# Kernel tuning notes

Measured on AMD Instinct MI355X. Metric: run time of the kernel, lower is better.

The kernel has to match this reference:

```python
import jax, jax.numpy as jnp
import numpy as np

B, S, D, E, K = 2, 4096, 1024, 8, 2

def setup_inputs() -> dict:
    key = jax.random.key(0)
    k1, k2, k3, k4, k5 = jax.random.split(key, 5)
    x = jax.random.normal(k1, (B, S, D), dtype=jnp.float32)
    expert_weights = jax.random.uniform(k2, (B, S, K), dtype=jnp.float32)
    top_k_indices = jax.random.randint(k3, (B, S, K), 0, E, dtype=jnp.int32)
    W = jax.random.normal(k4, (E, D, D), dtype=jnp.float32) * (1.0 / np.sqrt(D))
    b = jax.random.normal(k5, (E, D), dtype=jnp.float32) * 0.01
    return {"x": x, "expert_weights": expert_weights,
            "top_k_indices": top_k_indices, "W": W, "b": b}

def reference(x, expert_weights, top_k_indices, W, b):
    # Dense all-expert linear: [B,S,E,Dout]
    expert_outputs = jnp.einsum('bsd,edf->bsef', x, W) + b  # bias broadcasts over b,s
    # Gather the top-k expert outputs per token: [B,S,K,Dout]
    gathered = jnp.take_along_axis(expert_outputs, top_k_indices[:, :, :, None], axis=2)
    # Weighted combine over k
    output = jnp.sum(expert_weights[:, :, :, None] * gathered, axis=2)
    return output
```

## Files before the change

kernel.cpp:

```cpp
#include <hip/hip_runtime.h>
#include <hip/hip_bf16.h>
#include <cstdio>
#include <cstdint>

static constexpr int TOK = 8192;
static constexpr int DIM = 1024;
static constexpr int NEXP = 8;
static constexpr int NGRP = 16;
static constexpr int ROWS = TOK * 2;

typedef unsigned short u16;
typedef unsigned int u32;

using floatx4 = __attribute__((ext_vector_type(4))) float;
using bf16x8  = __attribute__((ext_vector_type(8))) __bf16;


__device__ __forceinline__ u16 f2bf(float f) {
  union { float f; u32 u; } v; v.f = f;
  u32 r = v.u + 0x7fffu + ((v.u >> 16) & 1u);
  return (u16)(r >> 16);
}

__device__ __forceinline__ float bf2f(u16 b) {
  union { u32 u; float f; } v; v.u = (u32)b << 16;
  return v.f;
}

__device__ __forceinline__ void gload_lds16(const void* g, void* l) {
  __builtin_amdgcn_global_load_lds(
      (const __attribute__((address_space(1))) void*)g,
      (__attribute__((address_space(3))) void*)l,
      16, 0, 0);
}

__global__ __launch_bounds__(1024)
void prep_kernel(const int* __restrict__ idx, const float* __restrict__ ew,
                 int* __restrict__ meta, int* __restrict__ tileMap,
                 int* __restrict__ tokList, float* __restrict__ wList) {
  __shared__ int cnt[NGRP];
  __shared__ int curL[NGRP];
  const int tid = threadIdx.x;
  if (tid < NGRP) cnt[tid] = 0;
  __syncthreads();
  int gloc[16];
#pragma unroll
  for (int j = 0; j < 16; ++j) {
    int i = tid + 1024 * j;
    int e = idx[i];
    int g = ((i & 1) << 3) | e;
    gloc[j] = g;
    atomicAdd(&cnt[g], 1);
  }
  __syncthreads();
  if (tid == 0) {
    int run = 0, t = 0, tk0 = 0;
    for (int g = 0; g < NGRP; ++g) {
      curL[g] = run;
      meta[g] = cnt[g];
      meta[16 + g] = run;
      int ntl = (cnt[g] + 127) >> 7;
      for (int m0 = 0; m0 < ntl; ++m0) tileMap[t++] = (g << 12) | m0;
      if (g == NEXP - 1) tk0 = t;
      run += cnt[g];
    }
    meta[48] = t;
    meta[49] = tk0;
  }
  __syncthreads();
#pragma unroll
  for (int j = 0; j < 16; ++j) {
    int i = tid + 1024 * j;
    int pos = atomicAdd(&curL[gloc[j]], 1);
    tokList[pos] = i >> 1;
    wList[pos] = ew[i];
  }
}

__global__ __launch_bounds__(256)
void gather_x_kernel(const float* __restrict__ x, const int* __restrict__ tokList,
                     u16* __restrict__ Abuf) {
  const int row = blockIdx.x;
  const int tok = tokList[row];
  const int tid = threadIdx.x;
  float4 v = reinterpret_cast<const float4*>(x + ((size_t)tok << 10))[tid];
  ushort4 o;
  o.x = f2bf(v.x); o.y = f2bf(v.y); o.z = f2bf(v.z); o.w = f2bf(v.w);
  reinterpret_cast<ushort4*>(Abuf + ((size_t)row << 10))[tid] = o;
}

__global__ void transpose_w_kernel(const float* __restrict__ W, u16* __restrict__ wt) {
  __shared__ u16 tile[32][33];
  const int e = blockIdx.z;
  const int f0 = blockIdx.x * 32, d0 = blockIdx.y * 32;
  const float* src = W + ((size_t)e << 20);
  u16* dst = wt + ((size_t)e << 20);
  const int tx = threadIdx.x, ty = threadIdx.y;
#pragma unroll
  for (int j = 0; j < 4; ++j) {
    int d = d0 + ty + 8 * j;
    tile[ty + 8 * j][tx] = f2bf(src[(size_t)d * DIM + f0 + tx]);
  }
  __syncthreads();
#pragma unroll
  for (int j = 0; j < 4; ++j) {
    int f = f0 + ty + 8 * j;
    dst[(size_t)f * DIM + d0 + tx] = tile[tx][ty + 8 * j];
  }
}

__global__ __launch_bounds__(256)
void moe_gemm_kernel(const u16* __restrict__ Abuf, const u16* __restrict__ wt,
                     const float* __restrict__ bias, const int* __restrict__ tokList,
                     const float* __restrict__ wList, const int* __restrict__ meta,
                     const int* __restrict__ tileMap, float* __restrict__ out,
                     u16* __restrict__ cbuf, int pass) {
  constexpr int BM = 128, BN = 128, BK = 64;
  const int chunk = gridDim.y;
  int lin = blockIdx.y * 8 + blockIdx.x;
  int swz = (lin & 7) * chunk + (lin >> 3);
  int tileIdx = swz >> 3, nt = swz & 7;

  int tBase = 0, tEnd = meta[48];
  const int tilesK0 = meta[49];
  if (pass == 0) tEnd = tilesK0;
  else if (pass == 1) tBase = tilesK0;
  tileIdx += tBase;
  if (tileIdx >= tEnd) return;

  const int tm = tileMap[tileIdx];
  const int g = tm >> 12, m0 = tm & 0xfff;
  const int e = g & (NEXP - 1);
  const int nrem = meta[g] - m0 * BM;
  const int listBase = meta[16 + g] + m0 * BM;

  __shared__ __align__(16) u16 As[BM * BK];
  __shared__ __align__(16) u16 Bs[BN * BK];

  const int tid = threadIdx.x;
  const int rowA = tid >> 3;
  const int chnk = tid & 7;
  const u16* wb = wt + ((size_t)e << 20);
  const u16* ab = Abuf + ((size_t)listBase << 10);

  const int wid = tid >> 6, lane = tid & 63;
  const int wm = (wid >> 1) * 64, wn = (wid & 1) * 64;
  const int lr = lane & 15, lg = lane >> 4;

  floatx4 acc[4][4];
#pragma unroll
  for (int i = 0; i < 4; ++i)
#pragma unroll
    for (int j = 0; j < 4; ++j) acc[i][j] = (floatx4){0.f, 0.f, 0.f, 0.f};

  for (int kt = 0; kt < DIM / BK; ++kt) {
    __syncthreads();
#pragma unroll
    for (int r = 0; r < 4; ++r) {
      const int row = rowA + 32 * r;
      gload_lds16(ab + ((size_t)row << 10) + kt * BK + chnk * 8,
                  &As[row * BK + chnk * 8]);
    }
#pragma unroll
    for (int r = 0; r < 4; ++r) {
      const int row = rowA + 32 * r;
      gload_lds16(wb + ((size_t)(nt * BN + row) << 10) + kt * BK + chnk * 8,
                  &Bs[row * BK + chnk * 8]);
    }
    asm volatile("s_waitcnt vmcnt(0)" ::: "memory");
    __syncthreads();

#pragma unroll
    for (int ks = 0; ks < 2; ++ks) {
      bf16x8 av[4], bv[4];
#pragma unroll
      for (int mi = 0; mi < 4; ++mi)
        av[mi] = *reinterpret_cast<const bf16x8*>(&As[(wm + mi * 16 + lr) * BK + ks * 32 + lg * 8]);
#pragma unroll
      for (int ni = 0; ni < 4; ++ni)
        bv[ni] = *reinterpret_cast<const bf16x8*>(&Bs[(wn + ni * 16 + lr) * BK + ks * 32 + lg * 8]);
#pragma unroll
      for (int mi = 0; mi < 4; ++mi)
#pragma unroll
        for (int ni = 0; ni < 4; ++ni)
          acc[mi][ni] = __builtin_amdgcn_mfma_f32_16x16x32_bf16(av[mi], bv[ni], acc[mi][ni], 0, 0, 0);
    }
  }

  const bool toCbuf = (pass < 0) && (g >= NEXP);
  const bool rmw = (pass == 1);
  const float* bp = bias + e * DIM;
#pragma unroll
  for (int mi = 0; mi < 4; ++mi) {
#pragma unroll
    for (int r = 0; r < 4; ++r) {
      const int rl = wm + mi * 16 + lg * 4 + r;
      if (rl < nrem) {
        const int   tok = tokList[listBase + rl];
        const float w   = wList[listBase + rl];
        const size_t rowOff = (size_t)tok << 10;
#pragma unroll
        for (int ni = 0; ni < 4; ++ni) {
          const int col = nt * BN + wn + ni * 16 + lr;
          const float v = w * (acc[mi][ni][r] + bp[col]);
          if (toCbuf)      cbuf[rowOff + col] = f2bf(v);
          else if (rmw)    out[rowOff + col] += v;
          else             out[rowOff + col] = v;
        }
      }
    }
  }
}

__global__ __launch_bounds__(256)
void combine_kernel(float* __restrict__ out, const u16* __restrict__ cbuf) {
  const int p = blockIdx.x * 256 + threadIdx.x;
  uint4 c = reinterpret_cast<const uint4*>(cbuf)[p];
  float4* o4 = reinterpret_cast<float4*>(out) + 2 * (size_t)p;
  float4 a = o4[0], b = o4[1];
  a.x += bf2f((u16)(c.x & 0xffff)); a.y += bf2f((u16)(c.x >> 16));
  a.z += bf2f((u16)(c.y & 0xffff)); a.w += bf2f((u16)(c.y >> 16));
  b.x += bf2f((u16)(c.z & 0xffff)); b.y += bf2f((u16)(c.z >> 16));
  b.z += bf2f((u16)(c.w & 0xffff)); b.w += bf2f((u16)(c.w >> 16));
  o4[0] = a; o4[1] = b;
}

extern "C" void kernel_launch(void* const* d_in, const int* in_sizes, int n_in,
                              void* d_out, int out_size, void* d_ws, size_t ws_size,
                              hipStream_t stream) {
  const float* x    = (const float*)d_in[0];
  const float* ew   = (const float*)d_in[1];
  const int*   idx  = (const int*)d_in[2];
  const float* W    = (const float*)d_in[3];
  const float* bias = (const float*)d_in[4];
  float* out = (float*)d_out;

  char* ws = (char*)d_ws;
  u16*   Abuf = (u16*)ws;
  u16*   wtp  = (u16*)(ws + ((size_t)32 << 20));
  u16*   cbuf = (u16*)(ws + ((size_t)48 << 20));

  const size_t needB = ((size_t)48 << 20) + (132 << 10);
  const size_t needA = ((size_t)64 << 20) + (132 << 10);
  if (ws_size < needB) {
    fprintf(stderr, "kernel_launch: ws_size %zu < needed %zu\n", ws_size, needB);
    return;
  }
  const bool modeA = (ws_size >= needA);
  char* tail = ws + (modeA ? ((size_t)64 << 20) : ((size_t)48 << 20));
  int*   tokList = (int*)tail;
  float* wList   = (float*)(tail + (64 << 10));
  int*   meta    = (int*)(tail + (128 << 10));
  int*   tileMap = (int*)(tail + (129 << 10));

  prep_kernel<<<1, 1024, 0, stream>>>(idx, ew, meta, tileMap, tokList, wList);
  gather_x_kernel<<<ROWS, 256, 0, stream>>>(x, tokList, Abuf);
  transpose_w_kernel<<<dim3(32, 32, 8), dim3(32, 8), 0, stream>>>(W, wtp);

  if (modeA) {
    moe_gemm_kernel<<<dim3(8, 144), 256, 0, stream>>>(
        Abuf, wtp, bias, tokList, wList, meta, tileMap, out, cbuf, -1);
    combine_kernel<<<TOK * DIM / 8 / 256, 256, 0, stream>>>(out, cbuf);
  } else {
    moe_gemm_kernel<<<dim3(8, 72), 256, 0, stream>>>(
        Abuf, wtp, bias, tokList, wList, meta, tileMap, out, nullptr, 0);
    moe_gemm_kernel<<<dim3(8, 72), 256, 0, stream>>>(
        Abuf, wtp, bias, tokList, wList, meta, tileMap, out, nullptr, 1);
  }
}
```

Baseline: 137.1 us.

## Replace two-pass combine with atomic-add epilogue and scatter-based gather

```diff
diff --git a/kernel.cpp b/kernel.cpp
--- a/kernel.cpp
+++ b/kernel.cpp
@@ -22,11 +22,6 @@
   return (u16)(r >> 16);
 }
 
-__device__ __forceinline__ float bf2f(u16 b) {
-  union { u32 u; float f; } v; v.u = (u32)b << 16;
-  return v.f;
-}
-
 __device__ __forceinline__ void gload_lds16(const void* g, void* l) {
   __builtin_amdgcn_global_load_lds(
       (const __attribute__((address_space(1))) void*)g,
@@ -37,56 +32,57 @@
 __global__ __launch_bounds__(1024)
 void prep_kernel(const int* __restrict__ idx, const float* __restrict__ ew,
                  int* __restrict__ meta, int* __restrict__ tileMap,
-                 int* __restrict__ tokList, float* __restrict__ wList) {
-  __shared__ int cnt[NGRP];
-  __shared__ int curL[NGRP];
+                 int* __restrict__ tokList, float* __restrict__ wList,
+                 int* __restrict__ posOf) {
+  __shared__ int cnt[NGRP], offS[NGRP], cur[NGRP], tbase[NGRP];
   const int tid = threadIdx.x;
   if (tid < NGRP) cnt[tid] = 0;
   __syncthreads();
-  int gloc[16];
+  int gl[16];
 #pragma unroll
   for (int j = 0; j < 16; ++j) {
     int i = tid + 1024 * j;
-    int e = idx[i];
-    int g = ((i & 1) << 3) | e;
-    gloc[j] = g;
+    int g = ((i & 1) << 3) | idx[i];
+    gl[j] = g;
     atomicAdd(&cnt[g], 1);
   }
   __syncthreads();
   if (tid == 0) {
-    int run = 0, t = 0, tk0 = 0;
+    int run = 0, t = 0;
     for (int g = 0; g < NGRP; ++g) {
-      curL[g] = run;
-      meta[g] = cnt[g];
-      meta[16 + g] = run;
-      int ntl = (cnt[g] + 127) >> 7;
-      for (int m0 = 0; m0 < ntl; ++m0) tileMap[t++] = (g << 12) | m0;
-      if (g == NEXP - 1) tk0 = t;
+      offS[g] = run; cur[g] = run; tbase[g] = t;
+      t += (cnt[g] + 127) >> 7;
       run += cnt[g];
     }
     meta[48] = t;
-    meta[49] = tk0;
-  }
-  __syncthreads();
+  }
+  __syncthreads();
+  if (tid < NGRP) {
+    meta[tid] = cnt[tid];
+    meta[16 + tid] = offS[tid];
+    int b = tbase[tid], n = (cnt[tid] + 127) >> 7;
+    for (int m0 = 0; m0 < n; ++m0) tileMap[b + m0] = (tid << 12) | m0;
+  }
 #pragma unroll
   for (int j = 0; j < 16; ++j) {
     int i = tid + 1024 * j;
-    int pos = atomicAdd(&curL[gloc[j]], 1);
+    int pos = atomicAdd(&cur[gl[j]], 1);
     tokList[pos] = i >> 1;
     wList[pos] = ew[i];
+    posOf[i] = pos;
   }
 }
 
 __global__ __launch_bounds__(256)
-void gather_x_kernel(const float* __restrict__ x, const int* __restrict__ tokList,
+void gather_x_kernel(const float* __restrict__ x, const int* __restrict__ posOf,
                      u16* __restrict__ Abuf) {
-  const int row = blockIdx.x;
-  const int tok = tokList[row];
-  const int tid = threadIdx.x;
-  float4 v = reinterpret_cast<const float4*>(x + ((size_t)tok << 10))[tid];
+  const int t = blockIdx.x, tid = threadIdx.x;
+  float4 v = reinterpret_cast<const float4*>(x + ((size_t)t << 10))[tid];
   ushort4 o;
   o.x = f2bf(v.x); o.y = f2bf(v.y); o.z = f2bf(v.z); o.w = f2bf(v.w);
-  reinterpret_cast<ushort4*>(Abuf + ((size_t)row << 10))[tid] = o;
+  const int p0 = posOf[2 * t], p1 = posOf[2 * t + 1];
+  reinterpret_cast<ushort4*>(Abuf + ((size_t)p0 << 10))[tid] = o;
+  reinterpret_cast<ushort4*>(Abuf + ((size_t)p1 << 10))[tid] = o;
 }
 
 __global__ void transpose_w_kernel(const float* __restrict__ W, u16* __restrict__ wt) {
@@ -110,23 +106,24 @@
 }
 
 __global__ __launch_bounds__(256)
+void zero_out_kernel(float4* __restrict__ out) {
+  const int i = blockIdx.x * 256 + threadIdx.x;
+#pragma unroll
+  for (int j = 0; j < 4; ++j)
+    out[i + j * 524288] = (float4){0.f, 0.f, 0.f, 0.f};
+}
+
+__global__ __launch_bounds__(256)
 void moe_gemm_kernel(const u16* __restrict__ Abuf, const u16* __restrict__ wt,
                      const float* __restrict__ bias, const int* __restrict__ tokList,
                      const float* __restrict__ wList, const int* __restrict__ meta,
-                     const int* __restrict__ tileMap, float* __restrict__ out,
-                     u16* __restrict__ cbuf, int pass) {
+                     const int* __restrict__ tileMap, float* __restrict__ out) {
   constexpr int BM = 128, BN = 128, BK = 64;
   const int chunk = gridDim.y;
   int lin = blockIdx.y * 8 + blockIdx.x;
   int swz = (lin & 7) * chunk + (lin >> 3);
   int tileIdx = swz >> 3, nt = swz & 7;
-
-  int tBase = 0, tEnd = meta[48];
-  const int tilesK0 = meta[49];
-  if (pass == 0) tEnd = tilesK0;
-  else if (pass == 1) tBase = tilesK0;
-  tileIdx += tBase;
-  if (tileIdx >= tEnd) return;
+  if (tileIdx >= meta[48]) return;
 
   const int tm = tileMap[tileIdx];
   const int g = tm >> 12, m0 = tm & 0xfff;
@@ -187,8 +184,6 @@
     }
   }
 
-  const bool toCbuf = (pass < 0) && (g >= NEXP);
-  const bool rmw = (pass == 1);
   const float* bp = bias + e * DIM;
 #pragma unroll
   for (int mi = 0; mi < 4; ++mi) {
@@ -198,31 +193,15 @@
       if (rl < nrem) {
         const int   tok = tokList[listBase + rl];
         const float w   = wList[listBase + rl];
-        const size_t rowOff = (size_t)tok << 10;
+        float* orow = out + ((size_t)tok << 10);
 #pragma unroll
         for (int ni = 0; ni < 4; ++ni) {
           const int col = nt * BN + wn + ni * 16 + lr;
-          const float v = w * (acc[mi][ni][r] + bp[col]);
-          if (toCbuf)      cbuf[rowOff + col] = f2bf(v);
-          else if (rmw)    out[rowOff + col] += v;
-          else             out[rowOff + col] = v;
+          unsafeAtomicAdd(&orow[col], w * (acc[mi][ni][r] + bp[col]));
         }
       }
     }
   }
-}
-
-__global__ __launch_bounds__(256)
-void combine_kernel(float* __restrict__ out, const u16* __restrict__ cbuf) {
-  const int p = blockIdx.x * 256 + threadIdx.x;
-  uint4 c = reinterpret_cast<const uint4*>(cbuf)[p];
-  float4* o4 = reinterpret_cast<float4*>(out) + 2 * (size_t)p;
-  float4 a = o4[0], b = o4[1];
-  a.x += bf2f((u16)(c.x & 0xffff)); a.y += bf2f((u16)(c.x >> 16));
-  a.z += bf2f((u16)(c.y & 0xffff)); a.w += bf2f((u16)(c.y >> 16));
-  b.x += bf2f((u16)(c.z & 0xffff)); b.y += bf2f((u16)(c.z >> 16));
-  b.z += bf2f((u16)(c.w & 0xffff)); b.w += bf2f((u16)(c.w >> 16));
-  o4[0] = a; o4[1] = b;
 }
 
 extern "C" void kernel_launch(void* const* d_in, const int* in_sizes, int n_in,
@@ -238,33 +217,23 @@
   char* ws = (char*)d_ws;
   u16*   Abuf = (u16*)ws;
   u16*   wtp  = (u16*)(ws + ((size_t)32 << 20));
-  u16*   cbuf = (u16*)(ws + ((size_t)48 << 20));
-
-  const size_t needB = ((size_t)48 << 20) + (132 << 10);
-  const size_t needA = ((size_t)64 << 20) + (132 << 10);
-  if (ws_size < needB) {
-    fprintf(stderr, "kernel_launch: ws_size %zu < needed %zu\n", ws_size, needB);
-    return;
-  }
-  const bool modeA = (ws_size >= needA);
-  char* tail = ws + (modeA ? ((size_t)64 << 20) : ((size_t)48 << 20));
+  char*  tail = ws + ((size_t)48 << 20);
   int*   tokList = (int*)tail;
   float* wList   = (float*)(tail + (64 << 10));
-  int*   meta    = (int*)(tail + (128 << 10));
-  int*   tileMap = (int*)(tail + (129 << 10));
-
-  prep_kernel<<<1, 1024, 0, stream>>>(idx, ew, meta, tileMap, tokList, wList);
-  gather_x_kernel<<<ROWS, 256, 0, stream>>>(x, tokList, Abuf);
+  int*   posOf   = (int*)(tail + (128 << 10));
+  int*   meta    = (int*)(tail + (192 << 10));
+  int*   tileMap = (int*)(tail + (193 << 10));
+
+  const size_t need = ((size_t)48 << 20) + (194 << 10);
+  if (ws_size < need) {
+    fprintf(stderr, "kernel_launch: ws_size %zu < needed %zu\n", ws_size, need);
+    return;
+  }
+
+  zero_out_kernel<<<2048, 256, 0, stream>>>((float4*)out);
+  prep_kernel<<<1, 1024, 0, stream>>>(idx, ew, meta, tileMap, tokList, wList, posOf);
+  gather_x_kernel<<<TOK, 256, 0, stream>>>(x, posOf, Abuf);
   transpose_w_kernel<<<dim3(32, 32, 8), dim3(32, 8), 0, stream>>>(W, wtp);
-
-  if (modeA) {
-    moe_gemm_kernel<<<dim3(8, 144), 256, 0, stream>>>(
-        Abuf, wtp, bias, tokList, wList, meta, tileMap, out, cbuf, -1);
-    combine_kernel<<<TOK * DIM / 8 / 256, 256, 0, stream>>>(out, cbuf);
-  } else {
-    moe_gemm_kernel<<<dim3(8, 72), 256, 0, stream>>>(
-        Abuf, wtp, bias, tokList, wList, meta, tileMap, out, nullptr, 0);
-    moe_gemm_kernel<<<dim3(8, 72), 256, 0, stream>>>(
-        Abuf, wtp, bias, tokList, wList, meta, tileMap, out, nullptr, 1);
-  }
-}
+  moe_gemm_kernel<<<dim3(8, 144), 256, 0, stream>>>(
+      Abuf, wtp, bias, tokList, wList, meta, tileMap, out);
+}
```

Result: slower. 155.2 us (+13.2%).

## Double-buffer MoE GEMM with 256x256 tiles, 512 threads, and scatter-style x gather

Applied to the files above, without the earlier changes.

```diff
diff --git a/kernel.cpp b/kernel.cpp
--- a/kernel.cpp
+++ b/kernel.cpp
@@ -7,7 +7,6 @@
 static constexpr int DIM = 1024;
 static constexpr int NEXP = 8;
 static constexpr int NGRP = 16;
-static constexpr int ROWS = TOK * 2;
 
 typedef unsigned short u16;
 typedef unsigned int u32;
@@ -37,30 +36,26 @@
 __global__ __launch_bounds__(1024)
 void prep_kernel(const int* __restrict__ idx, const float* __restrict__ ew,
                  int* __restrict__ meta, int* __restrict__ tileMap,
-                 int* __restrict__ tokList, float* __restrict__ wList) {
-  __shared__ int cnt[NGRP];
-  __shared__ int curL[NGRP];
+                 int* __restrict__ tokList, float* __restrict__ wList,
+                 int* __restrict__ posOf) {
+  __shared__ int cnt[NGRP], offS[NGRP], cur[NGRP], tbase[NGRP];
   const int tid = threadIdx.x;
   if (tid < NGRP) cnt[tid] = 0;
   __syncthreads();
-  int gloc[16];
+  int gl[16];
 #pragma unroll
   for (int j = 0; j < 16; ++j) {
     int i = tid + 1024 * j;
-    int e = idx[i];
-    int g = ((i & 1) << 3) | e;
-    gloc[j] = g;
+    int g = ((i & 1) << 3) | idx[i];
+    gl[j] = g;
     atomicAdd(&cnt[g], 1);
   }
   __syncthreads();
   if (tid == 0) {
     int run = 0, t = 0, tk0 = 0;
     for (int g = 0; g < NGRP; ++g) {
-      curL[g] = run;
-      meta[g] = cnt[g];
-      meta[16 + g] = run;
-      int ntl = (cnt[g] + 127) >> 7;
-      for (int m0 = 0; m0 < ntl; ++m0) tileMap[t++] = (g << 12) | m0;
+      offS[g] = run; cur[g] = run; tbase[g] = t;
+      t += (cnt[g] + 255) >> 8;
       if (g == NEXP - 1) tk0 = t;
       run += cnt[g];
     }
@@ -68,25 +63,32 @@
     meta[49] = tk0;
   }
   __syncthreads();
+  if (tid < NGRP) {
+    meta[tid] = cnt[tid];
+    meta[16 + tid] = offS[tid];
+    int b = tbase[tid], n = (cnt[tid] + 255) >> 8;
+    for (int m0 = 0; m0 < n; ++m0) tileMap[b + m0] = (tid << 12) | m0;
+  }
 #pragma unroll
   for (int j = 0; j < 16; ++j) {
     int i = tid + 1024 * j;
-    int pos = atomicAdd(&curL[gloc[j]], 1);
+    int pos = atomicAdd(&cur[gl[j]], 1);
     tokList[pos] = i >> 1;
     wList[pos] = ew[i];
+    posOf[i] = pos;
   }
 }
 
 __global__ __launch_bounds__(256)
-void gather_x_kernel(const float* __restrict__ x, const int* __restrict__ tokList,
+void gather_x_kernel(const float* __restrict__ x, const int* __restrict__ posOf,
                      u16* __restrict__ Abuf) {
-  const int row = blockIdx.x;
-  const int tok = tokList[row];
-  const int tid = threadIdx.x;
-  float4 v = reinterpret_cast<const float4*>(x + ((size_t)tok << 10))[tid];
+  const int t = blockIdx.x, tid = threadIdx.x;
+  float4 v = reinterpret_cast<const float4*>(x + ((size_t)t << 10))[tid];
   ushort4 o;
   o.x = f2bf(v.x); o.y = f2bf(v.y); o.z = f2bf(v.z); o.w = f2bf(v.w);
-  reinterpret_cast<ushort4*>(Abuf + ((size_t)row << 10))[tid] = o;
+  const int p0 = posOf[2 * t], p1 = posOf[2 * t + 1];
+  reinterpret_cast<ushort4*>(Abuf + ((size_t)p0 << 10))[tid] = o;
+  reinterpret_cast<ushort4*>(Abuf + ((size_t)p1 << 10))[tid] = o;
 }
 
 __global__ void transpose_w_kernel(const float* __restrict__ W, u16* __restrict__ wt) {
@@ -109,17 +111,20 @@
   }
 }
 
-__global__ __launch_bounds__(256)
+__global__ __launch_bounds__(512, 2)
 void moe_gemm_kernel(const u16* __restrict__ Abuf, const u16* __restrict__ wt,
                      const float* __restrict__ bias, const int* __restrict__ tokList,
                      const float* __restrict__ wList, const int* __restrict__ meta,
                      const int* __restrict__ tileMap, float* __restrict__ out,
                      u16* __restrict__ cbuf, int pass) {
-  constexpr int BM = 128, BN = 128, BK = 64;
-  const int chunk = gridDim.y;
-  int lin = blockIdx.y * 8 + blockIdx.x;
-  int swz = (lin & 7) * chunk + (lin >> 3);
-  int tileIdx = swz >> 3, nt = swz & 7;
+  constexpr int BM = 256, BN = 256, BK = 64;
+  constexpr int NKT = DIM / BK;
+  const int nwg = gridDim.x * gridDim.y;
+  const int lin = blockIdx.y * gridDim.x + blockIdx.x;
+  const int chunk = nwg >> 3;
+  const int swz = (lin & 7) * chunk + (lin >> 3);
+  int tileIdx = swz >> 2;
+  const int nt = swz & 3;
 
   int tBase = 0, tEnd = meta[48];
   const int tilesK0 = meta[49];
@@ -134,64 +139,87 @@
   const int nrem = meta[g] - m0 * BM;
   const int listBase = meta[16 + g] + m0 * BM;
 
-  __shared__ __align__(16) u16 As[BM * BK];
-  __shared__ __align__(16) u16 Bs[BN * BK];
+  __shared__ __align__(16) u16 As[2][BM * BK];
+  __shared__ __align__(16) u16 Bs[2][BN * BK];
 
   const int tid = threadIdx.x;
-  const int rowA = tid >> 3;
+  const int rowB = tid >> 3;
   const int chnk = tid & 7;
   const u16* wb = wt + ((size_t)e << 20);
   const u16* ab = Abuf + ((size_t)listBase << 10);
+  const size_t ntB = (size_t)nt * BN;
 
   const int wid = tid >> 6, lane = tid & 63;
-  const int wm = (wid >> 1) * 64, wn = (wid & 1) * 64;
+  const int wm = (wid >> 2) * 128;
+  const int wn = (wid & 3) * 64;
   const int lr = lane & 15, lg = lane >> 4;
 
-  floatx4 acc[4][4];
-#pragma unroll
-  for (int i = 0; i < 4; ++i)
+  floatx4 acc[8][4];
+#pragma unroll
+  for (int i = 0; i < 8; ++i)
 #pragma unroll
     for (int j = 0; j < 4; ++j) acc[i][j] = (floatx4){0.f, 0.f, 0.f, 0.f};
 
-  for (int kt = 0; kt < DIM / BK; ++kt) {
-    __syncthreads();
-#pragma unroll
-    for (int r = 0; r < 4; ++r) {
-      const int row = rowA + 32 * r;
-      gload_lds16(ab + ((size_t)row << 10) + kt * BK + chnk * 8,
-                  &As[row * BK + chnk * 8]);
-    }
-#pragma unroll
-    for (int r = 0; r < 4; ++r) {
-      const int row = rowA + 32 * r;
-      gload_lds16(wb + ((size_t)(nt * BN + row) << 10) + kt * BK + chnk * 8,
-                  &Bs[row * BK + chnk * 8]);
+#pragma unroll
+  for (int h = 0; h < 2; ++h)
+#pragma unroll
+    for (int r = 0; r < 2; ++r) {
+      const int row = h * 128 + rowB + 64 * r;
+      gload_lds16(ab + ((size_t)row << 10) + chnk * 8, &As[0][row * BK + chnk * 8]);
+      gload_lds16(wb + ((ntB + row) << 10) + chnk * 8, &Bs[0][row * BK + chnk * 8]);
+    }
+  asm volatile("s_waitcnt vmcnt(0)" ::: "memory");
+  __syncthreads();
+
+  for (int kt = 0; kt < NKT; ++kt) {
+    const int cb = kt & 1;
+#pragma unroll
+    for (int ph = 0; ph < 4; ++ph) {
+      if (kt < NKT - 1) {
+        const int h = ph & 1;
+        const size_t koff = (size_t)(kt + 1) * BK + chnk * 8;
+        if (ph < 2) {
+#pragma unroll
+          for (int r = 0; r < 2; ++r) {
+            const int row = h * 128 + rowB + 64 * r;
+            gload_lds16(ab + ((size_t)row << 10) + koff, &As[cb ^ 1][row * BK + chnk * 8]);
+          }
+        } else {
+#pragma unroll
+          for (int r = 0; r < 2; ++r) {
+            const int row = h * 128 + rowB + 64 * r;
+            gload_lds16(wb + ((ntB + row) << 10) + koff, &Bs[cb ^ 1][row * BK + chnk * 8]);
+          }
+        }
+      }
+      const int ks = ph >> 1, mh = ph & 1;
+      bf16x8 av[4], bv[4];
+#pragma unroll
+      for (int mi = 0; mi < 4; ++mi)
+        av[mi] = *reinterpret_cast<const bf16x8*>(
+            &As[cb][(wm + (mh * 4 + mi) * 16 + lr) * BK + ks * 32 + lg * 8]);
+#pragma unroll
+      for (int ni = 0; ni < 4; ++ni)
+        bv[ni] = *reinterpret_cast<const bf16x8*>(
+            &Bs[cb][(wn + ni * 16 + lr) * BK + ks * 32 + lg * 8]);
+      __builtin_amdgcn_s_setprio(1);
+#pragma unroll
+      for (int mi = 0; mi < 4; ++mi)
+#pragma unroll
+        for (int ni = 0; ni < 4; ++ni)
+          acc[mh * 4 + mi][ni] =
+              __builtin_amdgcn_mfma_f32_16x16x32_bf16(av[mi], bv[ni], acc[mh * 4 + mi][ni], 0, 0, 0);
+      __builtin_amdgcn_s_setprio(0);
     }
     asm volatile("s_waitcnt vmcnt(0)" ::: "memory");
     __syncthreads();
-
-#pragma unroll
-    for (int ks = 0; ks < 2; ++ks) {
-      bf16x8 av[4], bv[4];
-#pragma unroll
-      for (int mi = 0; mi < 4; ++mi)
-        av[mi] = *reinterpret_cast<const bf16x8*>(&As[(wm + mi * 16 + lr) * BK + ks * 32 + lg * 8]);
-#pragma unroll
-      for (int ni = 0; ni < 4; ++ni)
-        bv[ni] = *reinterpret_cast<const bf16x8*>(&Bs[(wn + ni * 16 + lr) * BK + ks * 32 + lg * 8]);
-#pragma unroll
-      for (int mi = 0; mi < 4; ++mi)
-#pragma unroll
-        for (int ni = 0; ni < 4; ++ni)
-          acc[mi][ni] = __builtin_amdgcn_mfma_f32_16x16x32_bf16(av[mi], bv[ni], acc[mi][ni], 0, 0, 0);
-    }
   }
 
   const bool toCbuf = (pass < 0) && (g >= NEXP);
   const bool rmw = (pass == 1);
   const float* bp = bias + e * DIM;
 #pragma unroll
-  for (int mi = 0; mi < 4; ++mi) {
+  for (int mi = 0; mi < 8; ++mi) {
 #pragma unroll
     for (int r = 0; r < 4; ++r) {
       const int rl = wm + mi * 16 + lg * 4 + r;
@@ -240,8 +268,8 @@
   u16*   wtp  = (u16*)(ws + ((size_t)32 << 20));
   u16*   cbuf = (u16*)(ws + ((size_t)48 << 20));
 
-  const size_t needB = ((size_t)48 << 20) + (132 << 10);
-  const size_t needA = ((size_t)64 << 20) + (132 << 10);
+  const size_t needB = ((size_t)48 << 20) + (194 << 10);
+  const size_t needA = ((size_t)64 << 20) + (194 << 10);
   if (ws_size < needB) {
     fprintf(stderr, "kernel_launch: ws_size %zu < needed %zu\n", ws_size, needB);
     return;
@@ -250,21 +278,22 @@
   char* tail = ws + (modeA ? ((size_t)64 << 20) : ((size_t)48 << 20));
   int*   tokList = (int*)tail;
   float* wList   = (float*)(tail + (64 << 10));
-  int*   meta    = (int*)(tail + (128 << 10));
-  int*   tileMap = (int*)(tail + (129 << 10));
-
-  prep_kernel<<<1, 1024, 0, stream>>>(idx, ew, meta, tileMap, tokList, wList);
-  gather_x_kernel<<<ROWS, 256, 0, stream>>>(x, tokList, Abuf);
+  int*   posOf   = (int*)(tail + (128 << 10));
+  int*   meta    = (int*)(tail + (192 << 10));
+  int*   tileMap = (int*)(tail + (193 << 10));
+
+  prep_kernel<<<1, 1024, 0, stream>>>(idx, ew, meta, tileMap, tokList, wList, posOf);
+  gather_x_kernel<<<TOK, 256, 0, stream>>>(x, posOf, Abuf);
   transpose_w_kernel<<<dim3(32, 32, 8), dim3(32, 8), 0, stream>>>(W, wtp);
 
   if (modeA) {
-    moe_gemm_kernel<<<dim3(8, 144), 256, 0, stream>>>(
+    moe_gemm_kernel<<<dim3(4, 80), 512, 0, stream>>>(
         Abuf, wtp, bias, tokList, wList, meta, tileMap, out, cbuf, -1);
     combine_kernel<<<TOK * DIM / 8 / 256, 256, 0, stream>>>(out, cbuf);
   } else {
-    moe_gemm_kernel<<<dim3(8, 72), 256, 0, stream>>>(
+    moe_gemm_kernel<<<dim3(4, 40), 512, 0, stream>>>(
         Abuf, wtp, bias, tokList, wList, meta, tileMap, out, nullptr, 0);
-    moe_gemm_kernel<<<dim3(8, 72), 256, 0, stream>>>(
+    moe_gemm_kernel<<<dim3(4, 40), 512, 0, stream>>>(
         Abuf, wtp, bias, tokList, wList, meta, tileMap, out, nullptr, 1);
   }
 }
```

Result: slower. 187.0 us (+36.4%).

## Scatter x rows by token, swizzle LDS tiles, parallelize tile map build

Applied to the files above, without the earlier changes.

```diff
diff --git a/kernel.cpp b/kernel.cpp
--- a/kernel.cpp
+++ b/kernel.cpp
@@ -7,7 +7,6 @@
 static constexpr int DIM = 1024;
 static constexpr int NEXP = 8;
 static constexpr int NGRP = 16;
-static constexpr int ROWS = TOK * 2;
 
 typedef unsigned short u16;
 typedef unsigned int u32;
@@ -37,30 +36,26 @@
 __global__ __launch_bounds__(1024)
 void prep_kernel(const int* __restrict__ idx, const float* __restrict__ ew,
                  int* __restrict__ meta, int* __restrict__ tileMap,
-                 int* __restrict__ tokList, float* __restrict__ wList) {
-  __shared__ int cnt[NGRP];
-  __shared__ int curL[NGRP];
+                 int* __restrict__ tokList, float* __restrict__ wList,
+                 int* __restrict__ posOf) {
+  __shared__ int cnt[NGRP], offS[NGRP], cur[NGRP], tbase[NGRP];
   const int tid = threadIdx.x;
   if (tid < NGRP) cnt[tid] = 0;
   __syncthreads();
-  int gloc[16];
+  int gl[16];
 #pragma unroll
   for (int j = 0; j < 16; ++j) {
     int i = tid + 1024 * j;
-    int e = idx[i];
-    int g = ((i & 1) << 3) | e;
-    gloc[j] = g;
+    int g = ((i & 1) << 3) | idx[i];
+    gl[j] = g;
     atomicAdd(&cnt[g], 1);
   }
   __syncthreads();
   if (tid == 0) {
     int run = 0, t = 0, tk0 = 0;
     for (int g = 0; g < NGRP; ++g) {
-      curL[g] = run;
-      meta[g] = cnt[g];
-      meta[16 + g] = run;
-      int ntl = (cnt[g] + 127) >> 7;
-      for (int m0 = 0; m0 < ntl; ++m0) tileMap[t++] = (g << 12) | m0;
+      offS[g] = run; cur[g] = run; tbase[g] = t;
+      t += (cnt[g] + 127) >> 7;
       if (g == NEXP - 1) tk0 = t;
       run += cnt[g];
     }
@@ -68,25 +63,32 @@
     meta[49] = tk0;
   }
   __syncthreads();
+  if (tid < NGRP) {
+    meta[tid] = cnt[tid];
+    meta[16 + tid] = offS[tid];
+    int b = tbase[tid], n = (cnt[tid] + 127) >> 7;
+    for (int m0 = 0; m0 < n; ++m0) tileMap[b + m0] = (tid << 12) | m0;
+  }
 #pragma unroll
   for (int j = 0; j < 16; ++j) {
     int i = tid + 1024 * j;
-    int pos = atomicAdd(&curL[gloc[j]], 1);
+    int pos = atomicAdd(&cur[gl[j]], 1);
     tokList[pos] = i >> 1;
     wList[pos] = ew[i];
+    posOf[i] = pos;
   }
 }
 
 __global__ __launch_bounds__(256)
-void gather_x_kernel(const float* __restrict__ x, const int* __restrict__ tokList,
+void gather_x_kernel(const float* __restrict__ x, const int* __restrict__ posOf,
                      u16* __restrict__ Abuf) {
-  const int row = blockIdx.x;
-  const int tok = tokList[row];
-  const int tid = threadIdx.x;
-  float4 v = reinterpret_cast<const float4*>(x + ((size_t)tok << 10))[tid];
+  const int t = blockIdx.x, tid = threadIdx.x;
+  float4 v = reinterpret_cast<const float4*>(x + ((size_t)t << 10))[tid];
   ushort4 o;
   o.x = f2bf(v.x); o.y = f2bf(v.y); o.z = f2bf(v.z); o.w = f2bf(v.w);
-  reinterpret_cast<ushort4*>(Abuf + ((size_t)row << 10))[tid] = o;
+  const int p0 = posOf[2 * t], p1 = posOf[2 * t + 1];
+  reinterpret_cast<ushort4*>(Abuf + ((size_t)p0 << 10))[tid] = o;
+  reinterpret_cast<ushort4*>(Abuf + ((size_t)p1 << 10))[tid] = o;
 }
 
 __global__ void transpose_w_kernel(const float* __restrict__ W, u16* __restrict__ wt) {
@@ -140,12 +142,14 @@
   const int tid = threadIdx.x;
   const int rowA = tid >> 3;
   const int chnk = tid & 7;
+  const int csw  = chnk ^ (rowA & 7);
   const u16* wb = wt + ((size_t)e << 20);
   const u16* ab = Abuf + ((size_t)listBase << 10);
 
   const int wid = tid >> 6, lane = tid & 63;
   const int wm = (wid >> 1) * 64, wn = (wid & 1) * 64;
   const int lr = lane & 15, lg = lane >> 4;
+  const int rx = lr & 7;
 
   floatx4 acc[4][4];
 #pragma unroll
@@ -158,13 +162,13 @@
 #pragma unroll
     for (int r = 0; r < 4; ++r) {
       const int row = rowA + 32 * r;
-      gload_lds16(ab + ((size_t)row << 10) + kt * BK + chnk * 8,
+      gload_lds16(ab + ((size_t)row << 10) + kt * BK + csw * 8,
                   &As[row * BK + chnk * 8]);
     }
 #pragma unroll
     for (int r = 0; r < 4; ++r) {
       const int row = rowA + 32 * r;
-      gload_lds16(wb + ((size_t)(nt * BN + row) << 10) + kt * BK + chnk * 8,
+      gload_lds16(wb + ((size_t)(nt * BN + row) << 10) + kt * BK + csw * 8,
                   &Bs[row * BK + chnk * 8]);
     }
     asm volatile("s_waitcnt vmcnt(0)" ::: "memory");
@@ -175,10 +179,12 @@
       bf16x8 av[4], bv[4];
 #pragma unroll
       for (int mi = 0; mi < 4; ++mi)
-        av[mi] = *reinterpret_cast<const bf16x8*>(&As[(wm + mi * 16 + lr) * BK + ks * 32 + lg * 8]);
+        av[mi] = *reinterpret_cast<const bf16x8*>(
+            &As[(wm + mi * 16 + lr) * BK + (((ks * 4 + lg) ^ rx)) * 8]);
 #pragma unroll
       for (int ni = 0; ni < 4; ++ni)
-        bv[ni] = *reinterpret_cast<const bf16x8*>(&Bs[(wn + ni * 16 + lr) * BK + ks * 32 + lg * 8]);
+        bv[ni] = *reinterpret_cast<const bf16x8*>(
+            &Bs[(wn + ni * 16 + lr) * BK + (((ks * 4 + lg) ^ rx)) * 8]);
 #pragma unroll
       for (int mi = 0; mi < 4; ++mi)
 #pragma unroll
@@ -240,8 +246,8 @@
   u16*   wtp  = (u16*)(ws + ((size_t)32 << 20));
   u16*   cbuf = (u16*)(ws + ((size_t)48 << 20));
 
-  const size_t needB = ((size_t)48 << 20) + (132 << 10);
-  const size_t needA = ((size_t)64 << 20) + (132 << 10);
+  const size_t needB = ((size_t)48 << 20) + (194 << 10);
+  const size_t needA = ((size_t)64 << 20) + (194 << 10);
   if (ws_size < needB) {
     fprintf(stderr, "kernel_launch: ws_size %zu < needed %zu\n", ws_size, needB);
     return;
@@ -250,11 +256,12 @@
   char* tail = ws + (modeA ? ((size_t)64 << 20) : ((size_t)48 << 20));
   int*   tokList = (int*)tail;
   float* wList   = (float*)(tail + (64 << 10));
-  int*   meta    = (int*)(tail + (128 << 10));
-  int*   tileMap = (int*)(tail + (129 << 10));
-
-  prep_kernel<<<1, 1024, 0, stream>>>(idx, ew, meta, tileMap, tokList, wList);
-  gather_x_kernel<<<ROWS, 256, 0, stream>>>(x, tokList, Abuf);
+  int*   posOf   = (int*)(tail + (128 << 10));
+  int*   meta    = (int*)(tail + (192 << 10));
+  int*   tileMap = (int*)(tail + (193 << 10));
+
+  prep_kernel<<<1, 1024, 0, stream>>>(idx, ew, meta, tileMap, tokList, wList, posOf);
+  gather_x_kernel<<<TOK, 256, 0, stream>>>(x, posOf, Abuf);
   transpose_w_kernel<<<dim3(32, 32, 8), dim3(32, 8), 0, stream>>>(W, wtp);
 
   if (modeA) {
```

After: 123.4 us. -10.0%, faster.
